# Kernel tuning notes

Hardware: AMD Instinct MI355X
Metric: run time of the kernel (lower is better)

The kernel has to match this reference:

```python
import jax, jax.numpy as jnp
import numpy as np

N = 50000        # graph nodes (= GRU batch)
E = N * 32       # edges
T_ENC = 48       # encoder length
T_F = 24         # forecast_len
H = 64           # GRU hidden size (both layers)


def setup_inputs() -> dict:
    key = jax.random.key(0)
    ks = jax.random.split(key, 26)
    p = lambda i, s: jax.random.normal(ks[i], s, dtype=jnp.float32) * 0.1
    src = jax.random.randint(ks[0], (E,), 0, N, dtype=jnp.int32)
    dst = (jnp.arange(E, dtype=jnp.int32) % N)  # every node gets 32 in-edges -> bincount > 0
    return {
        "encoder_input": jax.random.normal(ks[1], (N, T_ENC, 1), dtype=jnp.float32),
        "edge_attr": jax.random.uniform(ks[2], (E,), dtype=jnp.float32, minval=0.1, maxval=1.0),
        "stat_edge_index": jnp.stack([src, dst]),
        "gru0_wih": p(3, (3 * H, 1)), "gru0_whh": p(4, (3 * H, H)),
        "gru0_bih": p(5, (3 * H,)), "gru0_bhh": p(6, (3 * H,)),
        "gru1_wih": p(7, (3 * H, H)), "gru1_whh": p(8, (3 * H, H)),
        "gru1_bih": p(9, (3 * H,)), "gru1_bhh": p(10, (3 * H,)),
        "out1_w": p(11, (H, H)), "out1_b": p(12, (H,)),
        "out2_w": p(13, (1, H)), "out2_b": p(14, (1,)),
        "gnn_w1": p(15, (64, 14)), "gnn_b1": p(16, (64,)),
        "gnn_w2": p(17, (32, 64)), "gnn_b2": p(18, (32,)),
        "gnn_wout": p(19, (1, 32)), "gnn_bout": p(20, (1,)),
        "gnn_lin_w": p(21, (1, 1)),
        "out_param": jnp.float32(0.5),
    }


def _gru_seq(x, h0, wih, whh, bih, bhh):
    """PyTorch-convention GRU over x:[N,T,in] with h0:[N,H]. Gate order r,z,n."""
    def step(h, xt):
        gi = xt @ wih.T + bih
        gh = h @ whh.T + bhh
        ir, iz, i_n = jnp.split(gi, 3, axis=-1)
        hr, hz, h_n = jnp.split(gh, 3, axis=-1)
        r = jax.nn.sigmoid(ir + hr)
        z = jax.nn.sigmoid(iz + hz)
        n = jnp.tanh(i_n + r * h_n)
        h2 = (1.0 - z) * n + z * h
        return h2, h2
    hT, ys = jax.lax.scan(step, h0, jnp.swapaxes(x, 0, 1))
    return jnp.swapaxes(ys, 0, 1), hT


def reference(encoder_input, edge_attr, stat_edge_index,
              gru0_wih, gru0_whh, gru0_bih, gru0_bhh,
              gru1_wih, gru1_whh, gru1_bih, gru1_bhh,
              out1_w, out1_b, out2_w, out2_b,
              gnn_w1, gnn_b1, gnn_w2, gnn_b2, gnn_wout, gnn_bout, gnn_lin_w,
              out_param):
    src, dst = stat_edge_index[0], stat_edge_index[1]
    grus = [(gru0_wih, gru0_whh, gru0_bih, gru0_bhh),
            (gru1_wih, gru1_whh, gru1_bih, gru1_bhh)]

    def rnn(y, hidden):
        # RNNDecoder.forward (eval: dropout = identity)
        hs = []
        for i, (wih, whh, bih, bhh) in enumerate(grus):
            h0 = hidden[i] if hidden is not None else jnp.zeros((y.shape[0], whh.shape[1]), y.dtype)
            y, hT = _gru_seq(y, h0, wih, whh, bih, bhh)
            hs.append(hT)
        out = jax.nn.relu(y @ out1_w.T + out1_b) @ out2_w.T + out2_b
        return out, hs

    # bincount(edge_index[1], weights=edge_weight)
    norm = jax.ops.segment_sum(edge_attr, dst, num_segments=N)

    def gnn(x7):
        # CustomMessagePassing: gather -> MLP(14->64->32->1) -> edge-weight scale -> scatter-add -> normalize -> lin
        x_j = x7[src]                       # [E,7]
        x_i = x7[dst]                       # [E,7]
        m = jnp.concatenate([x_j, x_j - x_i], axis=1)   # [E,14]
        m = jax.nn.relu(m @ gnn_w1.T + gnn_b1)
        m = jax.nn.relu(m @ gnn_w2.T + gnn_b2)
        m = (m @ gnn_wout.T + gnn_bout) * edge_attr[:, None]   # [E,1]
        agg = jax.ops.segment_sum(m, dst, num_segments=N)       # [N,1]
        return (agg / norm[:, None]) @ gnn_lin_w.T              # update(): lin(out/norm)

    enc_output, hidden = rnn(encoder_input, None)   # [N,T_ENC,1]
    y_prev = enc_output[:, -1, :]                   # [N,1]
    buf6 = encoder_input[:, -6:, 0]                 # [N,6] rolling history
    s = jax.nn.sigmoid(out_param)

    def dec_step(carry, _):
        buf6, y_prev, h0, h1 = carry
        x7 = jnp.concatenate([buf6, y_prev], axis=1)   # cat(step_graph_input, y_prev)[:, -7:]
        diff = gnn(x7)                                  # [N,1]
        y_seq, hs = rnn(y_prev[:, None, :], [h0, h1])   # one GRU step
        out = s * y_seq[:, 0, :] + (1.0 - s) * diff
        return (x7[:, 1:], out, hs[0], hs[1]), out

    carry = (buf6, y_prev, hidden[0], hidden[1])
    _, ys = jax.lax.scan(dec_step, carry, None, length=T_F)   # [T_F,N,1]
    decoder_output = jnp.swapaxes(ys, 0, 1)                    # [N,T_F,1]
    return decoder_output, enc_output
```

## Files before the change

kernel.cpp:

```cpp
#include <hip/hip_runtime.h>
#include <hip/hip_cooperative_groups.h>

#define NN 50000
#define TE 48
#define TF 24
#define DEG 32
#define EE (NN*DEG)
#define NW 14
#define NPW 16
#define NPB (NW*NPW)
#define NBLK 224

#define F_W0H 0
#define F_W1I 24
#define F_W1H 48
#define F_O1W 72
#define F_GNN 80
#define DENSE_BYTES (88*1024)
#define SPARSE_OFF DENSE_BYTES
#define SPARSE_U32 576
#define W2_OFF (SPARSE_OFF + SPARSE_U32*4)
#define W2_ELEM_OFF (W2_OFF/2)
#define EXTRA_OFF (W2_OFF + 4096)
#define GBUF_BYTES (EXTRA_OFF + 512)

#define L_SPARSE_OFF DENSE_BYTES
#define L_EXTRA_OFF  (L_SPARSE_OFF + SPARSE_U32*4)
#define L_SCRATCH_OFF (L_EXTRA_OFF + 512)
#define WAVE_SCRATCH 2048
#define LDS_TOTAL (L_SCRATCH_OFF + NW*WAVE_SCRATCH)

typedef _Float16 f16;
typedef __attribute__((ext_vector_type(8))) _Float16 f16x8;
typedef __attribute__((ext_vector_type(2))) __fp16 fp16x2_builtin;
typedef __attribute__((ext_vector_type(4))) float f32x4;

__device__ __forceinline__ float frcp(float x) { return __builtin_amdgcn_rcpf(x); }
__device__ __forceinline__ float sigf(float x) { return frcp(1.f + __expf(-x)); }
__device__ __forceinline__ float tanhfast(float x) {
    float e = __expf(-2.f * fabsf(x));
    float r = (1.f - e) * frcp(1.f + e);
    return copysignf(r, x);
}
__device__ __forceinline__ f32x4 mf(f16x8 a, f16x8 b, f32x4 c) {
    return __builtin_amdgcn_mfma_f32_16x16x32_f16(a, b, c, 0, 0, 0);
}
__device__ __forceinline__ f16x8 ldfrag(const char* L, int f, int l) {
    return *(const f16x8*)(L + f * 1024 + l * 16);
}
__device__ __forceinline__ f16x8 spfrag(const unsigned* sp, int tt, int l, int g) {
    unsigned d = sp[tt * 16 + (l & 15)];
    if (g != 0) d = 0u;
    union { unsigned u; f16 h[2]; } c; c.u = d;
    f16x8 r = {};
    r[0] = c.h[0]; r[1] = c.h[1];
    return r;
}
__device__ __forceinline__ unsigned pk2(float a, float b) {
    fp16x2_builtin t = __builtin_amdgcn_cvt_pkrtz(a, b);
    union { fp16x2_builtin v; unsigned u; } c; c.v = t; return c.u;
}
__device__ __forceinline__ void upk2(unsigned u, float& a, float& b) {
    union { unsigned uu; f16 h[2]; } c; c.uu = u;
    a = (float)c.h[0]; b = (float)c.h[1];
}

struct Wctx {
    int l, g, n;
    char* S;
    const char* WL;
    const unsigned* SP;
    const float* XT;
};

__device__ __forceinline__ float gru16_step(const Wctx& W, float x,
    f16x8 (&h0B)[2], f16x8 (&h1B)[2], uint2 (&h0p)[4], uint2 (&h1p)[4])
{
    const f32x4 z4 = {0.f, 0.f, 0.f, 0.f};
    const int l = W.l, g = W.g, n = W.n;
    f16x8 xb = {};
    if (g == 0) { xb[0] = (f16)x; xb[1] = (f16)1.0f; }

    #pragma unroll
    for (int nt = 0; nt < 4; ++nt) {
        f32x4 aR = mf(spfrag(W.SP, nt, l, g), xb, z4);
        aR = mf(ldfrag(W.WL, F_W0H + nt * 2,     l), h0B[0], aR);
        aR = mf(ldfrag(W.WL, F_W0H + nt * 2 + 1, l), h0B[1], aR);
        f32x4 aZ = mf(spfrag(W.SP, 4 + nt, l, g), xb, z4);
        aZ = mf(ldfrag(W.WL, F_W0H + (4 + nt) * 2,     l), h0B[0], aZ);
        aZ = mf(ldfrag(W.WL, F_W0H + (4 + nt) * 2 + 1, l), h0B[1], aZ);
        f32x4 aNi = mf(spfrag(W.SP, 8 + nt, l, g), xb, z4);
        f32x4 aNh = mf(spfrag(W.SP, 12 + nt, l, g), xb, z4);
        aNh = mf(ldfrag(W.WL, F_W0H + (8 + nt) * 2,     l), h0B[0], aNh);
        aNh = mf(ldfrag(W.WL, F_W0H + (8 + nt) * 2 + 1, l), h0B[1], aNh);
        float ho[4], hn[4];
        upk2(h0p[nt].x, ho[0], ho[1]);
        upk2(h0p[nt].y, ho[2], ho[3]);
        #pragma unroll
        for (int r = 0; r < 4; ++r) {
            float rg = sigf(aR[r]);
            float zg = sigf(aZ[r]);
            float ng = tanhfast(aNi[r] + rg * aNh[r]);
            hn[r] = ng + zg * (ho[r] - ng);
        }
        h0p[nt].x = pk2(hn[0], hn[1]);
        h0p[nt].y = pk2(hn[2], hn[3]);
        *(uint2*)(W.S + n * 128 + (((2 * nt + (g >> 1)) ^ (n & 7)) * 16) + 8 * (g & 1)) = h0p[nt];
    }
    #pragma unroll
    for (int s = 0; s < 2; ++s)
        h0B[s] = *(const f16x8*)(W.S + n * 128 + (((4 * s + g) ^ (n & 7)) * 16));

    #pragma unroll
    for (int nt = 0; nt < 4; ++nt) {
        f32x4 aR = mf(spfrag(W.SP, 16 + nt, l, g), xb, z4);
        aR = mf(ldfrag(W.WL, F_W1I + nt * 2,     l), h0B[0], aR);
        aR = mf(ldfrag(W.WL, F_W1I + nt * 2 + 1, l), h0B[1], aR);
        aR = mf(ldfrag(W.WL, F_W1H + nt * 2,     l), h1B[0], aR);
        aR = mf(ldfrag(W.WL, F_W1H + nt * 2 + 1, l), h1B[1], aR);
        f32x4 aZ = mf(spfrag(W.SP, 20 + nt, l, g), xb, z4);
        aZ = mf(ldfrag(W.WL, F_W1I + (4 + nt) * 2,     l), h0B[0], aZ);
        aZ = mf(ldfrag(W.WL, F_W1I + (4 + nt) * 2 + 1, l), h0B[1], aZ);
        aZ = mf(ldfrag(W.WL, F_W1H + (4 + nt) * 2,     l), h1B[0], aZ);
        aZ = mf(ldfrag(W.WL, F_W1H + (4 + nt) * 2 + 1, l), h1B[1], aZ);
        f32x4 aNi = mf(spfrag(W.SP, 24 + nt, l, g), xb, z4);
        aNi = mf(ldfrag(W.WL, F_W1I + (8 + nt) * 2,     l), h0B[0], aNi);
        aNi = mf(ldfrag(W.WL, F_W1I + (8 + nt) * 2 + 1, l), h0B[1], aNi);
        f32x4 aNh = mf(spfrag(W.SP, 28 + nt, l, g), xb, z4);
        aNh = mf(ldfrag(W.WL, F_W1H + (8 + nt) * 2,     l), h1B[0], aNh);
        aNh = mf(ldfrag(W.WL, F_W1H + (8 + nt) * 2 + 1, l), h1B[1], aNh);
        float ho[4], hn[4];
        upk2(h1p[nt].x, ho[0], ho[1]);
        upk2(h1p[nt].y, ho[2], ho[3]);
        #pragma unroll
        for (int r = 0; r < 4; ++r) {
            float rg = sigf(aR[r]);
            float zg = sigf(aZ[r]);
            float ng = tanhfast(aNi[r] + rg * aNh[r]);
            hn[r] = ng + zg * (ho[r] - ng);
        }
        h1p[nt].x = pk2(hn[0], hn[1]);
        h1p[nt].y = pk2(hn[2], hn[3]);
        *(uint2*)(W.S + n * 128 + (((2 * nt + (g >> 1)) ^ (n & 7)) * 16) + 8 * (g & 1)) = h1p[nt];
    }
    #pragma unroll
    for (int s = 0; s < 2; ++s)
        h1B[s] = *(const f16x8*)(W.S + n * 128 + (((4 * s + g) ^ (n & 7)) * 16));

    float y = 0.f;
    #pragma unroll
    for (int nt = 0; nt < 4; ++nt) {
        f32x4 aH = mf(spfrag(W.SP, 32 + nt, l, g), xb, z4);
        aH = mf(ldfrag(W.WL, F_O1W + nt * 2,     l), h1B[0], aH);
        aH = mf(ldfrag(W.WL, F_O1W + nt * 2 + 1, l), h1B[1], aH);
        f32x4 ow = *(const f32x4*)(W.XT + 64 + nt * 16 + g * 4);
        #pragma unroll
        for (int r = 0; r < 4; ++r)
            y += fmaxf(aH[r], 0.f) * ow[r];
    }
    y += __shfl_xor(y, 16, 64);
    y += __shfl_xor(y, 32, 64);
    return y;
}

__device__ __forceinline__ void project_uv(const Wctx& W, const float (&win)[7],
    bool valid, int node, f16* __restrict__ ubw, f16x8& v0, f16x8& v1)
{
    const f32x4 z4 = {0.f, 0.f, 0.f, 0.f};
    const int g = W.g, n = W.n;
    f16x8 xw = {};
    if (g == 0) {
        #pragma unroll
        for (int j = 0; j < 7; ++j) xw[j] = (f16)win[j];
        xw[7] = (f16)1.0f;
    }
    #pragma unroll
    for (int mt = 0; mt < 4; ++mt) {
        f32x4 a = mf(ldfrag(W.WL, F_GNN + mt, W.l), xw, z4);
        uint2 wv; wv.x = pk2(a[0], a[1]); wv.y = pk2(a[2], a[3]);
        *(uint2*)(W.S + n * 128 + ((mt ^ (n & 3)) * 32) + g * 8) = wv;
    }
    {
        uint4 lo = *(const uint4*)(W.S + n * 128 + ((g ^ (n & 3)) * 32));
        uint4 hi = *(const uint4*)(W.S + n * 128 + ((g ^ (n & 3)) * 32) + 16);
        if (valid) {
            *(uint4*)&ubw[(size_t)node * 64 + g * 16]     = lo;
            *(uint4*)&ubw[(size_t)node * 64 + g * 16 + 8] = hi;
        }
    }
    #pragma unroll
    for (int mt = 0; mt < 4; ++mt) {
        f32x4 a = mf(ldfrag(W.WL, F_GNN + 4 + mt, W.l), xw, z4);
        uint2 wv; wv.x = pk2(a[0], a[1]); wv.y = pk2(a[2], a[3]);
        *(uint2*)(W.S + n * 128 + ((mt ^ (n & 3)) * 32) + g * 8) = wv;
    }
    v0 = *(const f16x8*)(W.S + n * 128 + ((((g >> 1))     ^ (n & 3)) * 32) + (g & 1) * 16);
    v1 = *(const f16x8*)(W.S + n * 128 + (((2 + (g >> 1)) ^ (n & 3)) * 32) + (g & 1) * 16);
}

__global__ __launch_bounds__(256)
void pack_weights(const float* __restrict__ w0i, const float* __restrict__ w0h,
                  const float* __restrict__ b0i, const float* __restrict__ b0h,
                  const float* __restrict__ w1i, const float* __restrict__ w1h,
                  const float* __restrict__ b1i, const float* __restrict__ b1h,
                  const float* __restrict__ o1w, const float* __restrict__ o1b,
                  const float* __restrict__ gw1, const float* __restrict__ gb1,
                  const float* __restrict__ gw2, const float* __restrict__ gb2,
                  const float* __restrict__ gwo, const float* __restrict__ o2w,
                  f16* __restrict__ wf, unsigned* __restrict__ sp)
{
    const int i = blockIdx.x * 256 + threadIdx.x;
    if (i < 92 * 64) {
        const int f = i >> 6, l = i & 63;
        const int lr = l & 15, g = l >> 4;
        f16x8 out = {};
        if (f < F_GNN) {
            const float* src; int fb;
            if (f < F_W1I)      { src = w0h; fb = f; }
            else if (f < F_W1H) { src = w1i; fb = f - F_W1I; }
            else if (f < F_O1W) { src = w1h; fb = f - F_W1H; }
            else                { src = o1w; fb = f - F_O1W; }
            const int nt = fb >> 1, s = fb & 1;
            const int row = nt * 16 + lr, k0 = s * 32 + g * 8;
            #pragma unroll
            for (int e = 0; e < 8; ++e) out[e] = (f16)src[row * 64 + k0 + e];
            *(f16x8*)&wf[f * 512 + l * 8] = out;
        } else if (f < 88) {
            const int mt = f - F_GNN;
            const int m = mt * 16 + lr;
            #pragma unroll
            for (int e = 0; e < 8; ++e) {
                int k = g * 8 + e; float v = 0.f;
                if (m < 64) {
                    if (k < 7) v = gw1[m * 14 + k] + gw1[m * 14 + 7 + k];
                    else if (k == 7) v = gb1[m];
                } else {
                    int mm = m - 64;
                    if (k < 7) v = -gw1[mm * 14 + 7 + k];
                }
                out[e] = (f16)v;
            }
            *(f16x8*)&wf[f * 512 + l * 8] = out;
        } else {
            const int fb = f - 88, nt = fb >> 1, s = fb & 1;
            const int row = nt * 16 + lr, k0 = s * 32 + g * 8;
            #pragma unroll
            for (int e = 0; e < 8; ++e) out[e] = (f16)gw2[row * 64 + k0 + e];
            *(f16x8*)&wf[W2_ELEM_OFF + fb * 512 + l * 8] = out;
        }
    } else {
        const int e = i - 92 * 64;
        if (e < SPARSE_U32) {
            const int tt = e >> 4, r16 = e & 15;
            float c0 = 0.f, c1 = 0.f;
            if (tt < 8)       { int row = tt*16 + r16;            c0 = w0i[row]; c1 = b0i[row] + b0h[row]; }
            else if (tt < 12) { int row = 128 + (tt-8)*16 + r16;  c0 = w0i[row]; c1 = b0i[row]; }
            else if (tt < 16) { int row = 128 + (tt-12)*16 + r16; c1 = b0h[row]; }
            else if (tt < 24) { int row = (tt-16)*16 + r16;       c1 = b1i[row] + b1h[row]; }
            else if (tt < 28) { int row = 128 + (tt-24)*16 + r16; c1 = b1i[row]; }
            else if (tt < 32) { int row = 128 + (tt-28)*16 + r16; c1 = b1h[row]; }
            else              { int row = (tt-32)*16 + r16;       c1 = o1b[row]; }
            union { f16 h[2]; unsigned u; } c;
            c.h[0] = (f16)c0; c.h[1] = (f16)c1;
            sp[e] = c.u;
        } else if (e < SPARSE_U32 + 128) {
            const int idx = e - SPARSE_U32;
            float v;
            if (idx < 32) v = gb2[idx];
            else if (idx < 64) v = gwo[idx - 32];
            else v = o2w[idx - 64];
            float* xf = (float*)((char*)wf + EXTRA_OFF);
            xf[idx] = v;
        }
    }
}

__global__ __launch_bounds__(896, 4)
void fused_kernel(const float* __restrict__ enc_in, const int* __restrict__ eidx,
                  const float* __restrict__ ea,
                  const float* __restrict__ o2b, const float* __restrict__ oparam,
                  const float* __restrict__ lin_w, const float* __restrict__ bo,
                  const f16* __restrict__ wfrag,
                  float* __restrict__ enc_out, float* __restrict__ dec_out,
                  f16* __restrict__ ub0, f16* __restrict__ ub1)
{
    extern __shared__ char smem[];
    const int tid = threadIdx.x;
    {
        uint4* d = (uint4*)smem;
        const uint4* s4 = (const uint4*)wfrag;
        for (int i = tid; i < L_EXTRA_OFF / 16; i += 896) d[i] = s4[i];
        if (tid < 32) {
            uint4* de = (uint4*)(smem + L_EXTRA_OFF);
            const uint4* se = (const uint4*)((const char*)wfrag + EXTRA_OFF);
            de[tid] = se[tid];
        }
    }
    __syncthreads();

    Wctx W;
    W.l = tid & 63;
    const int wid = __builtin_amdgcn_readfirstlane(tid >> 6);
    W.g = W.l >> 4; W.n = W.l & 15;
    W.WL = smem;
    W.SP = (const unsigned*)(smem + L_SPARSE_OFF);
    W.XT = (const float*)(smem + L_EXTRA_OFF);
    W.S  = smem + L_SCRATCH_OFF + wid * WAVE_SCRATCH;

    const f32x4 z4 = {0.f, 0.f, 0.f, 0.f};
    const int g = W.g;

    const int node = blockIdx.x * NPB + wid * NPW + W.n;
    const bool valid = node < NN;
    const int ndc = valid ? node : NN - 1;

    const float o2b0 = o2b[0];
    const float sv = sigf(oparam[0]);
    const float bo0 = bo[0];

    f16x8 Aw2[2][2];
    #pragma unroll
    for (int nj = 0; nj < 2; ++nj)
        #pragma unroll
        for (int s = 0; s < 2; ++s)
            Aw2[nj][s] = *(const f16x8*)&wfrag[W2_ELEM_OFF + (nj * 2 + s) * 512 + W.l * 8];

    float invc;
    {
        float nr = 0.f;
        #pragma unroll
        for (int kk = 0; kk < 8; ++kk) nr += ea[(size_t)(g * 8 + kk) * NN + ndc];
        nr += __shfl_xor(nr, 16, 64);
        nr += __shfl_xor(nr, 32, 64);
        invc = (1.f - sv) * lin_w[0] * frcp(nr);
    }

    f16x8 h0B[2] = {}, h1B[2] = {};
    uint2 h0p[4] = {}, h1p[4] = {};
    float win[7];
    float y = 0.f;
    {
        const float* pe = enc_in + (size_t)ndc * TE;
        for (int t = 0; t < TE; ++t) {
            y = gru16_step(W, pe[t], h0B, h1B, h0p, h1p) + o2b0;
            if (g == 0 && valid) enc_out[(size_t)node * TE + t] = y;
        }
        #pragma unroll
        for (int j = 0; j < 6; ++j) win[j] = pe[42 + j];
        win[6] = y;
    }
    f16x8 v0, v1;
    project_uv(W, win, valid, node, ub0, v0, v1);

    for (int t = 0; t < TF; ++t) {
        cooperative_groups::this_grid().sync();
        const f16* ub = (t & 1) ? ub1 : ub0;
        f16*      ubw = (t & 1) ? ub0 : ub1;

        f32x4 b2r0 = *(const f32x4*)(W.XT + 0  + g * 4);
        f32x4 b2r1 = *(const f32x4*)(W.XT + 16 + g * 4);
        f32x4 wor0 = *(const f32x4*)(W.XT + 32 + g * 4);
        f32x4 wor1 = *(const f32x4*)(W.XT + 48 + g * 4);
        float agg = 0.f;
        #pragma unroll 2
        for (int k = 0; k < DEG; ++k) {
            const int e = k * NN + ndc;
            const int srcn = eidx[e];
            const f16* up = ub + (size_t)srcn * 64;
            f16x8 u0 = *(const f16x8*)(up + g * 8);
            f16x8 u1 = *(const f16x8*)(up + 32 + g * 8);
            f16x8 m0, m1;
            #pragma unroll
            for (int j = 0; j < 8; ++j) {
                f16 a = u0[j] + v0[j]; m0[j] = a > (f16)0.f ? a : (f16)0.f;
                f16 b = u1[j] + v1[j]; m1[j] = b > (f16)0.f ? b : (f16)0.f;
            }
            f32x4 acc0 = mf(Aw2[0][0], m0, z4); acc0 = mf(Aw2[0][1], m1, acc0);
            f32x4 acc1 = mf(Aw2[1][0], m0, z4); acc1 = mf(Aw2[1][1], m1, acc1);
            float ps = 0.f;
            #pragma unroll
            for (int r = 0; r < 4; ++r)
                ps += fmaxf(acc0[r] + b2r0[r], 0.f) * wor0[r]
                    + fmaxf(acc1[r] + b2r1[r], 0.f) * wor1[r];
            ps += __shfl_xor(ps, 16, 64);
            ps += __shfl_xor(ps, 32, 64);
            agg += (ps + bo0) * ea[e];
        }

        y = gru16_step(W, win[6], h0B, h1B, h0p, h1p) + o2b0;

        float o = sv * y + agg * invc;
        if (g == 0 && valid) dec_out[(size_t)node * TF + t] = o;
        #pragma unroll
        for (int j = 0; j < 6; ++j) win[j] = win[j + 1];
        win[6] = o;

        if (t < TF - 1) project_uv(W, win, valid, node, ubw, v0, v1);
    }
}

extern "C" void kernel_launch(void* const* d_in, const int* in_sizes, int n_in,
                              void* d_out, int out_size, void* d_ws, size_t ws_size,
                              hipStream_t stream)
{
    const float* enc_in = (const float*)d_in[0];
    const float* ea     = (const float*)d_in[1];
    const int*   eidx   = (const int*)d_in[2];
    const float* w0i = (const float*)d_in[3];
    const float* w0h = (const float*)d_in[4];
    const float* b0i = (const float*)d_in[5];
    const float* b0h = (const float*)d_in[6];
    const float* w1i = (const float*)d_in[7];
    const float* w1h = (const float*)d_in[8];
    const float* b1i = (const float*)d_in[9];
    const float* b1h = (const float*)d_in[10];
    const float* o1w = (const float*)d_in[11];
    const float* o1b = (const float*)d_in[12];
    const float* o2w = (const float*)d_in[13];
    const float* o2b = (const float*)d_in[14];
    const float* gw1  = (const float*)d_in[15];
    const float* gb1  = (const float*)d_in[16];
    const float* gw2  = (const float*)d_in[17];
    const float* gb2  = (const float*)d_in[18];
    const float* gwo  = (const float*)d_in[19];
    const float* gbo  = (const float*)d_in[20];
    const float* glin = (const float*)d_in[21];
    const float* gop  = (const float*)d_in[22];

    float* dec_out = (float*)d_out;
    float* enc_out = dec_out + (size_t)NN * TF;

    char* ws = (char*)d_ws;
    f16*      wfrag = (f16*)ws;
    unsigned* sp    = (unsigned*)(ws + SPARSE_OFF);
    f16* ub0 = (f16*)(ws + ((GBUF_BYTES + 255) & ~255));
    f16* ub1 = ub0 + (size_t)NN * 64;

    (void)hipFuncSetAttribute((const void*)fused_kernel,
        hipFuncAttributeMaxDynamicSharedMemorySize, LDS_TOTAL);

    pack_weights<<<(92 * 64 + SPARSE_U32 + 128 + 255) / 256, 256, 0, stream>>>(
        w0i, w0h, b0i, b0h, w1i, w1h, b1i, b1h, o1w, o1b,
        gw1, gb1, gw2, gb2, gwo, o2w, wfrag, sp);

    void* args[] = {
        (void*)&enc_in, (void*)&eidx, (void*)&ea,
        (void*)&o2b, (void*)&gop, (void*)&glin, (void*)&gbo,
        (void*)&wfrag, (void*)&enc_out, (void*)&dec_out,
        (void*)&ub0, (void*)&ub1
    };
    (void)hipLaunchCooperativeKernel((const void*)fused_kernel, dim3(NBLK), dim3(896),
                                     args, LDS_TOTAL, stream);
}
```

Before: 2.410 ms.

## Split encoder and decoder into separate kernels and restructure GRU/GNN inner loops

Splits the fused cooperative kernel into an encoder kernel and a cooperative decoder kernel, passing final hidden states and history through global buffers. Blocks grow to 1024 threads (16 waves) across 196 blocks. The sparse bias fragments are pre-expanded to 64 lanes so the per-lane zeroing branch disappears. Layer-1 input and hidden accumulations become independent MFMA chains to shorten dependencies, and the edge loop now accumulates a weighted sum with one cross-lane reduction per step (bias folded in via the node degree) using vector f16 max. The split adds a kernel launch and global round-trips for hidden state, and changes occupancy and register pressure.

```diff
diff --git a/kernel.cpp b/kernel.cpp
--- a/kernel.cpp
+++ b/kernel.cpp
@@ -5,11 +5,10 @@
 #define TE 48
 #define TF 24
 #define DEG 32
-#define EE (NN*DEG)
-#define NW 14
+#define NW 16
 #define NPW 16
-#define NPB (NW*NPW)
-#define NBLK 224
+#define NPB 256
+#define NBLK 196
 
 #define F_W0H 0
 #define F_W1I 24
@@ -17,18 +16,17 @@
 #define F_O1W 72
 #define F_GNN 80
 #define DENSE_BYTES (88*1024)
-#define SPARSE_OFF DENSE_BYTES
-#define SPARSE_U32 576
-#define W2_OFF (SPARSE_OFF + SPARSE_U32*4)
-#define W2_ELEM_OFF (W2_OFF/2)
+#define SP64_OFF DENSE_BYTES
+#define SP64_BYTES (36*64*4)
+#define W2_OFF (SP64_OFF + SP64_BYTES)
+#define W2_ELEM (W2_OFF/2)
 #define EXTRA_OFF (W2_OFF + 4096)
 #define GBUF_BYTES (EXTRA_OFF + 512)
 
-#define L_SPARSE_OFF DENSE_BYTES
-#define L_EXTRA_OFF  (L_SPARSE_OFF + SPARSE_U32*4)
-#define L_SCRATCH_OFF (L_EXTRA_OFF + 512)
-#define WAVE_SCRATCH 2048
-#define LDS_TOTAL (L_SCRATCH_OFF + NW*WAVE_SCRATCH)
+#define L_XT_OFF (SP64_OFF + SP64_BYTES)
+#define L_SCR_OFF (L_XT_OFF + 512)
+#define WAVE_SCR 2048
+#define LDS_TOTAL (L_SCR_OFF + NW*WAVE_SCR)
 
 typedef _Float16 f16;
 typedef __attribute__((ext_vector_type(8))) _Float16 f16x8;
@@ -48,9 +46,8 @@
 __device__ __forceinline__ f16x8 ldfrag(const char* L, int f, int l) {
     return *(const f16x8*)(L + f * 1024 + l * 16);
 }
-__device__ __forceinline__ f16x8 spfrag(const unsigned* sp, int tt, int l, int g) {
-    unsigned d = sp[tt * 16 + (l & 15)];
-    if (g != 0) d = 0u;
+__device__ __forceinline__ f16x8 spfrag64(const unsigned* sp, int tt, int l) {
+    unsigned d = sp[tt * 64 + l];
     union { unsigned u; f16 h[2]; } c; c.u = d;
     f16x8 r = {};
     r[0] = c.h[0]; r[1] = c.h[1];
@@ -73,24 +70,33 @@
     const float* XT;
 };
 
+__device__ __forceinline__ void transp(const Wctx& W, const uint2 (&hp)[4], f16x8 (&hB)[2]) {
+    #pragma unroll
+    for (int nt = 0; nt < 4; ++nt)
+        *(uint2*)(W.S + W.n * 128 + (((2 * nt + (W.g >> 1)) ^ (W.n & 7)) * 16) + 8 * (W.g & 1)) = hp[nt];
+    #pragma unroll
+    for (int s = 0; s < 2; ++s)
+        hB[s] = *(const f16x8*)(W.S + W.n * 128 + (((4 * s + W.g) ^ (W.n & 7)) * 16));
+}
+
 __device__ __forceinline__ float gru16_step(const Wctx& W, float x,
     f16x8 (&h0B)[2], f16x8 (&h1B)[2], uint2 (&h0p)[4], uint2 (&h1p)[4])
 {
     const f32x4 z4 = {0.f, 0.f, 0.f, 0.f};
-    const int l = W.l, g = W.g, n = W.n;
+    const int l = W.l, g = W.g;
     f16x8 xb = {};
     if (g == 0) { xb[0] = (f16)x; xb[1] = (f16)1.0f; }
 
     #pragma unroll
     for (int nt = 0; nt < 4; ++nt) {
-        f32x4 aR = mf(spfrag(W.SP, nt, l, g), xb, z4);
+        f32x4 aR = mf(spfrag64(W.SP, nt, l), xb, z4);
         aR = mf(ldfrag(W.WL, F_W0H + nt * 2,     l), h0B[0], aR);
         aR = mf(ldfrag(W.WL, F_W0H + nt * 2 + 1, l), h0B[1], aR);
-        f32x4 aZ = mf(spfrag(W.SP, 4 + nt, l, g), xb, z4);
+        f32x4 aZ = mf(spfrag64(W.SP, 4 + nt, l), xb, z4);
         aZ = mf(ldfrag(W.WL, F_W0H + (4 + nt) * 2,     l), h0B[0], aZ);
         aZ = mf(ldfrag(W.WL, F_W0H + (4 + nt) * 2 + 1, l), h0B[1], aZ);
-        f32x4 aNi = mf(spfrag(W.SP, 8 + nt, l, g), xb, z4);
-        f32x4 aNh = mf(spfrag(W.SP, 12 + nt, l, g), xb, z4);
+        f32x4 aNi = mf(spfrag64(W.SP, 8 + nt, l), xb, z4);
+        f32x4 aNh = mf(spfrag64(W.SP, 12 + nt, l), xb, z4);
         aNh = mf(ldfrag(W.WL, F_W0H + (8 + nt) * 2,     l), h0B[0], aNh);
         aNh = mf(ldfrag(W.WL, F_W0H + (8 + nt) * 2 + 1, l), h0B[1], aNh);
         float ho[4], hn[4];
@@ -105,28 +111,25 @@
         }
         h0p[nt].x = pk2(hn[0], hn[1]);
         h0p[nt].y = pk2(hn[2], hn[3]);
-        *(uint2*)(W.S + n * 128 + (((2 * nt + (g >> 1)) ^ (n & 7)) * 16) + 8 * (g & 1)) = h0p[nt];
-    }
-    #pragma unroll
-    for (int s = 0; s < 2; ++s)
-        h0B[s] = *(const f16x8*)(W.S + n * 128 + (((4 * s + g) ^ (n & 7)) * 16));
+    }
+    transp(W, h0p, h0B);
 
     #pragma unroll
     for (int nt = 0; nt < 4; ++nt) {
-        f32x4 aR = mf(spfrag(W.SP, 16 + nt, l, g), xb, z4);
-        aR = mf(ldfrag(W.WL, F_W1I + nt * 2,     l), h0B[0], aR);
-        aR = mf(ldfrag(W.WL, F_W1I + nt * 2 + 1, l), h0B[1], aR);
-        aR = mf(ldfrag(W.WL, F_W1H + nt * 2,     l), h1B[0], aR);
-        aR = mf(ldfrag(W.WL, F_W1H + nt * 2 + 1, l), h1B[1], aR);
-        f32x4 aZ = mf(spfrag(W.SP, 20 + nt, l, g), xb, z4);
-        aZ = mf(ldfrag(W.WL, F_W1I + (4 + nt) * 2,     l), h0B[0], aZ);
-        aZ = mf(ldfrag(W.WL, F_W1I + (4 + nt) * 2 + 1, l), h0B[1], aZ);
-        aZ = mf(ldfrag(W.WL, F_W1H + (4 + nt) * 2,     l), h1B[0], aZ);
-        aZ = mf(ldfrag(W.WL, F_W1H + (4 + nt) * 2 + 1, l), h1B[1], aZ);
-        f32x4 aNi = mf(spfrag(W.SP, 24 + nt, l, g), xb, z4);
+        f32x4 aRa = mf(spfrag64(W.SP, 16 + nt, l), xb, z4);
+        aRa = mf(ldfrag(W.WL, F_W1I + nt * 2,     l), h0B[0], aRa);
+        aRa = mf(ldfrag(W.WL, F_W1I + nt * 2 + 1, l), h0B[1], aRa);
+        f32x4 aRb = mf(ldfrag(W.WL, F_W1H + nt * 2, l), h1B[0], z4);
+        aRb = mf(ldfrag(W.WL, F_W1H + nt * 2 + 1,   l), h1B[1], aRb);
+        f32x4 aZa = mf(spfrag64(W.SP, 20 + nt, l), xb, z4);
+        aZa = mf(ldfrag(W.WL, F_W1I + (4 + nt) * 2,     l), h0B[0], aZa);
+        aZa = mf(ldfrag(W.WL, F_W1I + (4 + nt) * 2 + 1, l), h0B[1], aZa);
+        f32x4 aZb = mf(ldfrag(W.WL, F_W1H + (4 + nt) * 2, l), h1B[0], z4);
+        aZb = mf(ldfrag(W.WL, F_W1H + (4 + nt) * 2 + 1,   l), h1B[1], aZb);
+        f32x4 aNi = mf(spfrag64(W.SP, 24 + nt, l), xb, z4);
         aNi = mf(ldfrag(W.WL, F_W1I + (8 + nt) * 2,     l), h0B[0], aNi);
         aNi = mf(ldfrag(W.WL, F_W1I + (8 + nt) * 2 + 1, l), h0B[1], aNi);
-        f32x4 aNh = mf(spfrag(W.SP, 28 + nt, l, g), xb, z4);
+        f32x4 aNh = mf(spfrag64(W.SP, 28 + nt, l), xb, z4);
         aNh = mf(ldfrag(W.WL, F_W1H + (8 + nt) * 2,     l), h1B[0], aNh);
         aNh = mf(ldfrag(W.WL, F_W1H + (8 + nt) * 2 + 1, l), h1B[1], aNh);
         float ho[4], hn[4];
@@ -134,26 +137,23 @@
         upk2(h1p[nt].y, ho[2], ho[3]);
         #pragma unroll
         for (int r = 0; r < 4; ++r) {
-            float rg = sigf(aR[r]);
-            float zg = sigf(aZ[r]);
+            float rg = sigf(aRa[r] + aRb[r]);
+            float zg = sigf(aZa[r] + aZb[r]);
             float ng = tanhfast(aNi[r] + rg * aNh[r]);
             hn[r] = ng + zg * (ho[r] - ng);
         }
         h1p[nt].x = pk2(hn[0], hn[1]);
         h1p[nt].y = pk2(hn[2], hn[3]);
-        *(uint2*)(W.S + n * 128 + (((2 * nt + (g >> 1)) ^ (n & 7)) * 16) + 8 * (g & 1)) = h1p[nt];
-    }
-    #pragma unroll
-    for (int s = 0; s < 2; ++s)
-        h1B[s] = *(const f16x8*)(W.S + n * 128 + (((4 * s + g) ^ (n & 7)) * 16));
+    }
+    transp(W, h1p, h1B);
 
     float y = 0.f;
     #pragma unroll
     for (int nt = 0; nt < 4; ++nt) {
-        f32x4 aH = mf(spfrag(W.SP, 32 + nt, l, g), xb, z4);
+        f32x4 aH = mf(spfrag64(W.SP, 32 + nt, l), xb, z4);
         aH = mf(ldfrag(W.WL, F_O1W + nt * 2,     l), h1B[0], aH);
         aH = mf(ldfrag(W.WL, F_O1W + nt * 2 + 1, l), h1B[1], aH);
-        f32x4 ow = *(const f32x4*)(W.XT + 64 + nt * 16 + g * 4);
+        f32x4 ow = *(const f32x4*)(W.XT + 64 + nt * 16 + W.g * 4);
         #pragma unroll
         for (int r = 0; r < 4; ++r)
             y += fmaxf(aH[r], 0.f) * ow[r];
@@ -196,6 +196,18 @@
     }
     v0 = *(const f16x8*)(W.S + n * 128 + ((((g >> 1))     ^ (n & 3)) * 32) + (g & 1) * 16);
     v1 = *(const f16x8*)(W.S + n * 128 + (((2 + (g >> 1)) ^ (n & 3)) * 32) + (g & 1) * 16);
+}
+
+__device__ __forceinline__ void stage_all(char* smem, const f16* wfrag, int tid) {
+    uint4* d = (uint4*)smem;
+    const uint4* s4 = (const uint4*)wfrag;
+    for (int i = tid; i < L_XT_OFF / 16; i += 1024) d[i] = s4[i];
+    if (tid < 32) {
+        uint4* de = (uint4*)(smem + L_XT_OFF);
+        const uint4* se = (const uint4*)((const char*)wfrag + EXTRA_OFF);
+        de[tid] = se[tid];
+    }
+    __syncthreads();
 }
 
 __global__ __launch_bounds__(256)
@@ -207,7 +219,7 @@
                   const float* __restrict__ gw1, const float* __restrict__ gb1,
                   const float* __restrict__ gw2, const float* __restrict__ gb2,
                   const float* __restrict__ gwo, const float* __restrict__ o2w,
-                  f16* __restrict__ wf, unsigned* __restrict__ sp)
+                  f16* __restrict__ wf)
 {
     const int i = blockIdx.x * 256 + threadIdx.x;
     if (i < 92 * 64) {
@@ -246,12 +258,14 @@
             const int row = nt * 16 + lr, k0 = s * 32 + g * 8;
             #pragma unroll
             for (int e = 0; e < 8; ++e) out[e] = (f16)gw2[row * 64 + k0 + e];
-            *(f16x8*)&wf[W2_ELEM_OFF + fb * 512 + l * 8] = out;
-        }
-    } else {
+            *(f16x8*)&wf[W2_ELEM + fb * 512 + l * 8] = out;
+        }
+    } else if (i < 92 * 64 + 36 * 64) {
         const int e = i - 92 * 64;
-        if (e < SPARSE_U32) {
-            const int tt = e >> 4, r16 = e & 15;
+        const int tt = e >> 6, l = e & 63;
+        unsigned val = 0u;
+        if (l < 16) {
+            const int r16 = l;
             float c0 = 0.f, c1 = 0.f;
             if (tt < 8)       { int row = tt*16 + r16;            c0 = w0i[row]; c1 = b0i[row] + b0h[row]; }
             else if (tt < 12) { int row = 128 + (tt-8)*16 + r16;  c0 = w0i[row]; c1 = b0i[row]; }
@@ -260,59 +274,96 @@
             else if (tt < 28) { int row = 128 + (tt-24)*16 + r16; c1 = b1i[row]; }
             else if (tt < 32) { int row = 128 + (tt-28)*16 + r16; c1 = b1h[row]; }
             else              { int row = (tt-32)*16 + r16;       c1 = o1b[row]; }
-            union { f16 h[2]; unsigned u; } c;
-            c.h[0] = (f16)c0; c.h[1] = (f16)c1;
-            sp[e] = c.u;
-        } else if (e < SPARSE_U32 + 128) {
-            const int idx = e - SPARSE_U32;
-            float v;
-            if (idx < 32) v = gb2[idx];
-            else if (idx < 64) v = gwo[idx - 32];
-            else v = o2w[idx - 64];
-            float* xf = (float*)((char*)wf + EXTRA_OFF);
-            xf[idx] = v;
-        }
-    }
-}
-
-__global__ __launch_bounds__(896, 4)
-void fused_kernel(const float* __restrict__ enc_in, const int* __restrict__ eidx,
-                  const float* __restrict__ ea,
-                  const float* __restrict__ o2b, const float* __restrict__ oparam,
-                  const float* __restrict__ lin_w, const float* __restrict__ bo,
-                  const f16* __restrict__ wfrag,
-                  float* __restrict__ enc_out, float* __restrict__ dec_out,
-                  f16* __restrict__ ub0, f16* __restrict__ ub1)
+            val = pk2(c0, c1);
+        }
+        ((unsigned*)((char*)wf + SP64_OFF))[tt * 64 + l] = val;
+    } else if (i < 92 * 64 + 36 * 64 + 128) {
+        const int idx = i - 92 * 64 - 36 * 64;
+        float v;
+        if (idx < 32) v = gb2[idx];
+        else if (idx < 64) v = gwo[idx - 32];
+        else v = o2w[idx - 64];
+        float* xf = (float*)((char*)wf + EXTRA_OFF);
+        xf[idx] = v;
+    }
+}
+
+__global__ __launch_bounds__(1024, 4)
+void enc_kernel(const float* __restrict__ enc_in, const float* __restrict__ o2b,
+                const f16* __restrict__ wfrag, float* __restrict__ enc_out,
+                uint2* __restrict__ hsb, float* __restrict__ hist)
 {
     extern __shared__ char smem[];
     const int tid = threadIdx.x;
-    {
-        uint4* d = (uint4*)smem;
-        const uint4* s4 = (const uint4*)wfrag;
-        for (int i = tid; i < L_EXTRA_OFF / 16; i += 896) d[i] = s4[i];
-        if (tid < 32) {
-            uint4* de = (uint4*)(smem + L_EXTRA_OFF);
-            const uint4* se = (const uint4*)((const char*)wfrag + EXTRA_OFF);
-            de[tid] = se[tid];
-        }
-    }
-    __syncthreads();
+    stage_all(smem, wfrag, tid);
 
     Wctx W;
     W.l = tid & 63;
     const int wid = __builtin_amdgcn_readfirstlane(tid >> 6);
     W.g = W.l >> 4; W.n = W.l & 15;
     W.WL = smem;
-    W.SP = (const unsigned*)(smem + L_SPARSE_OFF);
-    W.XT = (const float*)(smem + L_EXTRA_OFF);
-    W.S  = smem + L_SCRATCH_OFF + wid * WAVE_SCRATCH;
-
-    const f32x4 z4 = {0.f, 0.f, 0.f, 0.f};
-    const int g = W.g;
+    W.SP = (const unsigned*)(smem + SP64_OFF);
+    W.XT = (const float*)(smem + L_XT_OFF);
+    W.S  = smem + L_SCR_OFF + wid * WAVE_SCR;
 
     const int node = blockIdx.x * NPB + wid * NPW + W.n;
     const bool valid = node < NN;
     const int ndc = valid ? node : NN - 1;
+    const float o2b0 = o2b[0];
+
+    f16x8 h0B[2] = {}, h1B[2] = {};
+    uint2 h0p[4] = {}, h1p[4] = {};
+    const float* pe = enc_in + (size_t)ndc * TE;
+    float y = 0.f;
+    for (int t = 0; t < TE; ++t) {
+        y = gru16_step(W, pe[t], h0B, h1B, h0p, h1p) + o2b0;
+        if (W.g == 0 && valid) enc_out[(size_t)node * TE + t] = y;
+    }
+    {
+        uint2* hb0 = hsb + ((size_t)ndc * 2 + 0) * 16 + W.g * 4;
+        uint2* hb1 = hsb + ((size_t)ndc * 2 + 1) * 16 + W.g * 4;
+        uint4 a0 = {h0p[0].x, h0p[0].y, h0p[1].x, h0p[1].y};
+        uint4 a1 = {h0p[2].x, h0p[2].y, h0p[3].x, h0p[3].y};
+        uint4 b0 = {h1p[0].x, h1p[0].y, h1p[1].x, h1p[1].y};
+        uint4 b1 = {h1p[2].x, h1p[2].y, h1p[3].x, h1p[3].y};
+        if (valid) {
+            *(uint4*)&hb0[0] = a0; *(uint4*)&hb0[2] = a1;
+            *(uint4*)&hb1[0] = b0; *(uint4*)&hb1[2] = b1;
+        }
+    }
+    if (W.g == 0 && valid) {
+        #pragma unroll
+        for (int j = 0; j < 6; ++j) hist[(size_t)node * 8 + j] = pe[42 + j];
+        hist[(size_t)node * 8 + 6] = y;
+    }
+}
+
+__global__ __launch_bounds__(1024, 4)
+void dec_kernel(const int* __restrict__ eidx, const float* __restrict__ ea,
+                const float* __restrict__ o2b, const float* __restrict__ oparam,
+                const float* __restrict__ lin_w, const float* __restrict__ bo,
+                const f16* __restrict__ wfrag, float* __restrict__ dec_out,
+                const uint2* __restrict__ hsb, const float* __restrict__ hist,
+                f16* __restrict__ ub0, f16* __restrict__ ub1)
+{
+    extern __shared__ char smem[];
+    const int tid = threadIdx.x;
+    stage_all(smem, wfrag, tid);
+
+    Wctx W;
+    W.l = tid & 63;
+    const int wid = __builtin_amdgcn_readfirstlane(tid >> 6);
+    W.g = W.l >> 4; W.n = W.l & 15;
+    W.WL = smem;
+    W.SP = (const unsigned*)(smem + SP64_OFF);
+    W.XT = (const float*)(smem + L_XT_OFF);
+    W.S  = smem + L_SCR_OFF + wid * WAVE_SCR;
+
+    const f32x4 z4 = {0.f, 0.f, 0.f, 0.f};
+    const int g = W.g;
+    const int node = blockIdx.x * NPB + wid * NPW + W.n;
+    const bool valid = node < NN;
+    const int ndc = valid ? node : NN - 1;
 
     const float o2b0 = o2b[0];
     const float sv = sigf(oparam[0]);
@@ -323,9 +374,9 @@
     for (int nj = 0; nj < 2; ++nj)
         #pragma unroll
         for (int s = 0; s < 2; ++s)
-            Aw2[nj][s] = *(const f16x8*)&wfrag[W2_ELEM_OFF + (nj * 2 + s) * 512 + W.l * 8];
-
-    float invc;
+            Aw2[nj][s] = *(const f16x8*)&wfrag[W2_ELEM + (nj * 2 + s) * 512 + W.l * 8];
+
+    float invc, nb0;
     {
         float nr = 0.f;
         #pragma unroll
@@ -333,22 +384,28 @@
         nr += __shfl_xor(nr, 16, 64);
         nr += __shfl_xor(nr, 32, 64);
         invc = (1.f - sv) * lin_w[0] * frcp(nr);
-    }
-
-    f16x8 h0B[2] = {}, h1B[2] = {};
-    uint2 h0p[4] = {}, h1p[4] = {};
+        nb0 = bo0 * nr;
+    }
+    f32x4 b2r0 = *(const f32x4*)(W.XT + 0  + g * 4);
+    f32x4 b2r1 = *(const f32x4*)(W.XT + 16 + g * 4);
+    f32x4 wor0 = *(const f32x4*)(W.XT + 32 + g * 4);
+    f32x4 wor1 = *(const f32x4*)(W.XT + 48 + g * 4);
+
+    uint2 h0p[4], h1p[4];
+    {
+        const uint2* hb0 = hsb + ((size_t)ndc * 2 + 0) * 16 + g * 4;
+        const uint2* hb1 = hsb + ((size_t)ndc * 2 + 1) * 16 + g * 4;
+        #pragma unroll
+        for (int nt = 0; nt < 4; ++nt) { h0p[nt] = hb0[nt]; h1p[nt] = hb1[nt]; }
+    }
+    f16x8 h0B[2], h1B[2];
+    transp(W, h0p, h0B);
+    transp(W, h1p, h1B);
+
     float win[7];
-    float y = 0.f;
-    {
-        const float* pe = enc_in + (size_t)ndc * TE;
-        for (int t = 0; t < TE; ++t) {
-            y = gru16_step(W, pe[t], h0B, h1B, h0p, h1p) + o2b0;
-            if (g == 0 && valid) enc_out[(size_t)node * TE + t] = y;
-        }
-        #pragma unroll
-        for (int j = 0; j < 6; ++j) win[j] = pe[42 + j];
-        win[6] = y;
-    }
+    #pragma unroll
+    for (int j = 0; j < 7; ++j) win[j] = (g == 0) ? hist[(size_t)ndc * 8 + j] : 0.f;
+
     f16x8 v0, v1;
     project_uv(W, win, valid, node, ub0, v0, v1);
 
@@ -357,24 +414,17 @@
         const f16* ub = (t & 1) ? ub1 : ub0;
         f16*      ubw = (t & 1) ? ub0 : ub1;
 
-        f32x4 b2r0 = *(const f32x4*)(W.XT + 0  + g * 4);
-        f32x4 b2r1 = *(const f32x4*)(W.XT + 16 + g * 4);
-        f32x4 wor0 = *(const f32x4*)(W.XT + 32 + g * 4);
-        f32x4 wor1 = *(const f32x4*)(W.XT + 48 + g * 4);
-        float agg = 0.f;
-        #pragma unroll 2
+        float S = 0.f;
+        #pragma unroll 8
         for (int k = 0; k < DEG; ++k) {
             const int e = k * NN + ndc;
             const int srcn = eidx[e];
             const f16* up = ub + (size_t)srcn * 64;
             f16x8 u0 = *(const f16x8*)(up + g * 8);
             f16x8 u1 = *(const f16x8*)(up + 32 + g * 8);
-            f16x8 m0, m1;
-            #pragma unroll
-            for (int j = 0; j < 8; ++j) {
-                f16 a = u0[j] + v0[j]; m0[j] = a > (f16)0.f ? a : (f16)0.f;
-                f16 b = u1[j] + v1[j]; m1[j] = b > (f16)0.f ? b : (f16)0.f;
-            }
+            f16x8 zh = {};
+            f16x8 m0 = __builtin_elementwise_max((f16x8)(u0 + v0), zh);
+            f16x8 m1 = __builtin_elementwise_max((f16x8)(u1 + v1), zh);
             f32x4 acc0 = mf(Aw2[0][0], m0, z4); acc0 = mf(Aw2[0][1], m1, acc0);
             f32x4 acc1 = mf(Aw2[1][0], m0, z4); acc1 = mf(Aw2[1][1], m1, acc1);
             float ps = 0.f;
@@ -382,19 +432,18 @@
             for (int r = 0; r < 4; ++r)
                 ps += fmaxf(acc0[r] + b2r0[r], 0.f) * wor0[r]
                     + fmaxf(acc1[r] + b2r1[r], 0.f) * wor1[r];
-            ps += __shfl_xor(ps, 16, 64);
-            ps += __shfl_xor(ps, 32, 64);
-            agg += (ps + bo0) * ea[e];
-        }
-
-        y = gru16_step(W, win[6], h0B, h1B, h0p, h1p) + o2b0;
-
-        float o = sv * y + agg * invc;
+            S = fmaf(ps, ea[e], S);
+        }
+        S += __shfl_xor(S, 16, 64);
+        S += __shfl_xor(S, 32, 64);
+        const float aggT = S + nb0;
+
+        float y = gru16_step(W, win[6], h0B, h1B, h0p, h1p) + o2b0;
+        float o = sv * y + aggT * invc;
         if (g == 0 && valid) dec_out[(size_t)node * TF + t] = o;
         #pragma unroll
         for (int j = 0; j < 6; ++j) win[j] = win[j + 1];
         win[6] = o;
-
         if (t < TF - 1) project_uv(W, win, valid, node, ubw, v0, v1);
     }
 }
@@ -431,24 +480,28 @@
     float* enc_out = dec_out + (size_t)NN * TF;
 
     char* ws = (char*)d_ws;
-    f16*      wfrag = (f16*)ws;
-    unsigned* sp    = (unsigned*)(ws + SPARSE_OFF);
-    f16* ub0 = (f16*)(ws + ((GBUF_BYTES + 255) & ~255));
-    f16* ub1 = ub0 + (size_t)NN * 64;
-
-    (void)hipFuncSetAttribute((const void*)fused_kernel,
+    f16* wfrag = (f16*)ws;
+    char* p = ws + ((GBUF_BYTES + 255) & ~255);
+    f16*   ub0  = (f16*)p;    p += (size_t)NN * 64 * 2;
+    f16*   ub1  = (f16*)p;    p += (size_t)NN * 64 * 2;
+    uint2* hsb  = (uint2*)p;  p += (size_t)NN * 32 * 8;
+    float* hist = (float*)p;  p += (size_t)NN * 8 * 4;
+
+    (void)hipFuncSetAttribute((const void*)enc_kernel,
         hipFuncAttributeMaxDynamicSharedMemorySize, LDS_TOTAL);
-
-    pack_weights<<<(92 * 64 + SPARSE_U32 + 128 + 255) / 256, 256, 0, stream>>>(
-        w0i, w0h, b0i, b0h, w1i, w1h, b1i, b1h, o1w, o1b,
-        gw1, gb1, gw2, gb2, gwo, o2w, wfrag, sp);
+    (void)hipFuncSetAttribute((const void*)dec_kernel,
+        hipFuncAttributeMaxDynamicSharedMemorySize, LDS_TOTAL);
+
+    pack_weights<<<33, 256, 0, stream>>>(w0i, w0h, b0i, b0h, w1i, w1h, b1i, b1h,
+                                         o1w, o1b, gw1, gb1, gw2, gb2, gwo, o2w, wfrag);
+
+    enc_kernel<<<NBLK, 1024, LDS_TOTAL, stream>>>(enc_in, o2b, wfrag, enc_out, hsb, hist);
 
     void* args[] = {
-        (void*)&enc_in, (void*)&eidx, (void*)&ea,
-        (void*)&o2b, (void*)&gop, (void*)&glin, (void*)&gbo,
-        (void*)&wfrag, (void*)&enc_out, (void*)&dec_out,
+        (void*)&eidx, (void*)&ea, (void*)&o2b, (void*)&gop, (void*)&glin, (void*)&gbo,
+        (void*)&wfrag, (void*)&dec_out, (void*)&hsb, (void*)&hist,
         (void*)&ub0, (void*)&ub1
     };
-    (void)hipLaunchCooperativeKernel((const void*)fused_kernel, dim3(NBLK), dim3(896),
+    (void)hipLaunchCooperativeKernel((const void*)dec_kernel, dim3(NBLK), dim3(1024),
                                      args, LDS_TOTAL, stream);
 }
```

Measured after the change: 2.487 ms. +3.2%, slower.
